# Optimization experiments

Measured on AMD Instinct MI355X. Metric: run time of the kernel, lower is better.

The kernel has to match this reference:

```python
import jax, jax.numpy as jnp
import numpy as np


def setup_inputs() -> dict:
    key = jax.random.key(0)
    ks = jax.random.split(key, 5)
    B, H, S, C, Dh = 2, 16, 2048, 2048, 64
    HID = H * Dh
    return {
        "q": jax.random.normal(ks[0], (B, H, S, Dh), dtype=jnp.float32),
        "k": jax.random.normal(ks[1], (B, H, C + S, Dh), dtype=jnp.float32),
        "v": jax.random.normal(ks[2], (B, H, C + S, Dh), dtype=jnp.float32),
        "memory_length": 256,
        "W": jax.random.normal(ks[3], (HID, HID), dtype=jnp.float32) / np.sqrt(HID),
        "b": jax.random.normal(ks[4], (HID,), dtype=jnp.float32) * 0.01,
    }


def _build_mask(S, KV, memory_length):
    # KV = CACHE_LEN + S; columns >= CACHE_LEN + memory_length are restricted.
    C = KV - S
    rows = jnp.arange(S)[:, None]          # query position in [0, S)
    cols = jnp.arange(KV)[None, :]         # key position in [0, KV)
    restricted = cols >= (C + memory_length)
    # memory rows (< memory_length) never see restricted cols;
    # other rows: strictly-upper-triangular masking (col - (C+mem) > row - mem)
    mem_row = rows < memory_length
    future = (cols - (C + memory_length)) > (rows - memory_length)
    return (restricted & (mem_row | future))  # bool [S, KV], True = masked


def reference(q, k, v, memory_length, W, b):
    B, H, S, Dh = q.shape
    KV = k.shape[2]
    HID = H * Dh
    scale = 1.0 / np.sqrt(Dh).astype(np.float32)
    scores = jnp.einsum('bhsd,bhtd->bhst', q, k) * scale   # [B,H,S,KV]
    mask2d = _build_mask(S, KV, memory_length)             # [S,KV] bool
    scores = jnp.where(mask2d[None, None], -jnp.inf, scores)
    attn_w = jax.nn.softmax(scores, axis=-1)
    attn = jnp.einsum('bhst,bhtd->bshd', attn_w, v).reshape(B, S, HID)
    out = attn @ W.T + b
    # torch module returns full [B,H,S,KV] float mask of 0/1
    mask_full = jnp.broadcast_to(mask2d.astype(q.dtype), (B, H, S, KV))
    return out, mask_full
```

## Files before the change

kernel.cpp:

```cpp
#include <hip/hip_runtime.h>
#include <hip/hip_bf16.h>
#include <math.h>

typedef __bf16 bf16;
typedef __bf16 bf16x4 __attribute__((ext_vector_type(4)));
typedef __bf16 bf16x8 __attribute__((ext_vector_type(8)));
typedef float f32x4 __attribute__((ext_vector_type(4)));

#define MFMA(a, b, c) __builtin_amdgcn_mfma_f32_16x16x32_bf16((a), (b), (c), 0, 0, 0)

constexpr int Bb  = 2;
constexpr int Hh  = 16;
constexpr int Ss  = 2048;
constexpr int KVv = 4096;
constexpr int Dd  = 64;
constexpr int Cc  = KVv - Ss;
constexpr int HID = Hh * Dd;

constexpr float QSCL = 0.125f * 1.44269504088896340736f;

constexpr size_t MASK_F4   = (size_t)Bb * Hh * Ss * KVv / 4;
constexpr size_t SCR_BYTES = 16777216ull + 16777216ull + 2097152ull + 8388608ull;
constexpr size_t M2_F4     = MASK_F4 - (2097152ull + 8388608ull) / 16;
constexpr size_t M1_F4     = 50000000;

__device__ __forceinline__ void write_mask_range(
    float* __restrict__ mout, int mem, size_t lo, size_t hi,
    int mblk, int nmblk, int tid, int nthr)
{
    const int R = Cc + mem;
    const size_t stride = (size_t)nmblk * nthr;
    for (size_t i = lo + (size_t)mblk * nthr + tid; i < hi; i += stride) {
        size_t flat = i * 4;
        int t = (int)(flat & (size_t)(KVv - 1));
        int s = (int)((flat >> 12) & (size_t)(Ss - 1));
        int thr = (s < mem) ? R : (s + Cc + 1);
        f32x4 vv;
        vv[0] = (float)(t >= thr);
        vv[1] = (float)(t + 1 >= thr);
        vv[2] = (float)(t + 2 >= thr);
        vv[3] = (float)(t + 3 >= thr);
        __builtin_nontemporal_store(vv, (f32x4*)(mout + flat));
    }
}

__global__ __launch_bounds__(256) void cvt_kernel(
    const float* __restrict__ K, const float* __restrict__ W,
    bf16* __restrict__ Kb, bf16* __restrict__ Wb)
{
    const size_t nK4 = (size_t)Bb * Hh * KVv * Dd / 4;
    const size_t nW4 = (size_t)HID * HID / 4;
    const size_t total = nK4 + nW4;
    const size_t stride = (size_t)gridDim.x * blockDim.x;
    for (size_t i = (size_t)blockIdx.x * blockDim.x + threadIdx.x; i < total; i += stride) {
        float4 x = (i < nK4) ? ((const float4*)K)[i] : ((const float4*)W)[i - nK4];
        bf16x4 t;
        t[0] = (bf16)x.x; t[1] = (bf16)x.y; t[2] = (bf16)x.z; t[3] = (bf16)x.w;
        if (i < nK4) ((bf16x4*)Kb)[i] = t;
        else         ((bf16x4*)Wb)[i - nK4] = t;
    }
}

__global__ __launch_bounds__(256) void vT_kernel(
    const float* __restrict__ V, bf16* __restrict__ Vt)
{
    __shared__ __align__(16) bf16 T[64][72];
    const int bh = blockIdx.y;
    const int t0 = blockIdx.x * 64;
    const int row = threadIdx.x >> 2;
    const int cg  = threadIdx.x & 3;

    const float* vb = V + (size_t)bh * KVv * Dd + (size_t)(t0 + row) * Dd + cg * 16;
    float4 x0 = ((const float4*)vb)[0];
    float4 x1 = ((const float4*)vb)[1];
    float4 x2 = ((const float4*)vb)[2];
    float4 x3 = ((const float4*)vb)[3];
    float xs[16] = {x0.x,x0.y,x0.z,x0.w, x1.x,x1.y,x1.z,x1.w,
                    x2.x,x2.y,x2.z,x2.w, x3.x,x3.y,x3.z,x3.w};
#pragma unroll
    for (int j = 0; j < 16; ++j)
        T[cg * 16 + j][row] = (bf16)xs[j];
    __syncthreads();

    const int d = row;
    bf16* o = Vt + (size_t)bh * Dd * KVv + (size_t)d * KVv + t0 + cg * 16;
    bf16x8 a0 = *(const bf16x8*)&T[d][cg * 16];
    bf16x8 a1 = *(const bf16x8*)&T[d][cg * 16 + 8];
    ((bf16x8*)o)[0] = a0;
    ((bf16x8*)o)[1] = a1;
}

template <bool MASKED>
__device__ __forceinline__ void kv_tile(
    int t0, const bf16* __restrict__ kb_p, const bf16* __restrict__ vt_p,
    const bf16x8 qa[2], const int thr[4], int tid, int lr, int lg,
    bf16 (*__restrict__ Klds)[72], bf16 (*__restrict__ Vlds)[72],
    bf16 (*__restrict__ Pw)[72], f32x4 acco[4], float lsum[4])
{
    {
        const int row = tid >> 3, c8 = tid & 7;
        bf16x8 kx = *(const bf16x8*)(kb_p + (size_t)(t0 + row) * Dd + c8 * 8);
        bf16x8 vx = *(const bf16x8*)(vt_p + (size_t)row * KVv + t0 + c8 * 8);
        *(bf16x8*)&Klds[row][c8 * 8] = kx;
        *(bf16x8*)&Vlds[row][c8 * 8] = vx;
    }
    __syncthreads();

    f32x4 accs[4];
#pragma unroll
    for (int kg = 0; kg < 4; ++kg) accs[kg] = (f32x4){0.f, 0.f, 0.f, 0.f};
    __builtin_amdgcn_s_setprio(1);
#pragma unroll
    for (int ks = 0; ks < 2; ++ks) {
#pragma unroll
        for (int kg = 0; kg < 4; ++kg) {
            bf16x8 kf = *(const bf16x8*)&Klds[kg * 16 + lr][ks * 32 + lg * 8];
            accs[kg] = MFMA(qa[ks], kf, accs[kg]);
        }
    }
    __builtin_amdgcn_s_setprio(0);

#pragma unroll
    for (int r = 0; r < 4; ++r) {
#pragma unroll
        for (int kg = 0; kg < 4; ++kg) {
            float sl = accs[kg][r];
            if (MASKED) {
                int tcol = t0 + kg * 16 + lr;
                sl = (tcol < thr[r]) ? sl : -1e30f;
            }
            accs[kg][r] = __builtin_amdgcn_exp2f(sl);
        }
        lsum[r] += (accs[0][r] + accs[1][r]) + (accs[2][r] + accs[3][r]);
#pragma unroll
        for (int kg = 0; kg < 4; ++kg)
            Pw[lg * 4 + r][kg * 16 + lr] = (bf16)accs[kg][r];
    }
    asm volatile("s_waitcnt lgkmcnt(0)" ::: "memory");

    __builtin_amdgcn_s_setprio(1);
#pragma unroll
    for (int ks = 0; ks < 2; ++ks) {
        bf16x8 pa = *(const bf16x8*)&Pw[lr][ks * 32 + lg * 8];
#pragma unroll
        for (int dg = 0; dg < 4; ++dg) {
            bf16x8 vf = *(const bf16x8*)&Vlds[dg * 16 + lr][ks * 32 + lg * 8];
            acco[dg] = MFMA(pa, vf, acco[dg]);
        }
    }
    __builtin_amdgcn_s_setprio(0);
    __syncthreads();
}

__global__ __launch_bounds__(512) void fused_attn_kernel(
    const float* __restrict__ q, const bf16* __restrict__ Kb,
    const bf16* __restrict__ Vtb, const int* __restrict__ memp,
    bf16* __restrict__ attnb, float* __restrict__ mout)
{
    __shared__ __align__(16) bf16 Klds[64][72];
    __shared__ __align__(16) bf16 Vlds[64][72];
    __shared__ __align__(16) bf16 Plds[8][16][72];

    const int fid = blockIdx.x;
    const int mem = *memp;
    if (fid >= 512) {
        write_mask_range(mout, mem, 0, M1_F4, fid - 512, gridDim.x - 512,
                         threadIdx.x, 512);
        return;
    }
    const int xcd = fid & 7;
    const int slot = fid >> 3;
    const int qblk = slot & 15;
    const int bh = (slot >> 4) * 8 + xcd;

    const int tid = threadIdx.x;
    const int w  = tid >> 6;
    const int l  = tid & 63;
    const int lr = l & 15;
    const int lg = l >> 4;
    const int q0 = qblk * 128;
    const int R = Cc + mem;

    const float* qp   = q   + (size_t)bh * Ss * Dd;
    const bf16*  kb_p = Kb  + (size_t)bh * KVv * Dd;
    const bf16*  vt_p = Vtb + (size_t)bh * Dd * KVv;

    const int qrow = q0 + w * 16 + lr;
    bf16x8 qa[2];
#pragma unroll
    for (int ks = 0; ks < 2; ++ks) {
        const float* p8 = qp + (size_t)qrow * Dd + ks * 32 + lg * 8;
        float4 x0 = *(const float4*)p8;
        float4 x1 = *(const float4*)(p8 + 4);
        bf16x8 a;
        a[0] = (bf16)(x0.x * QSCL); a[1] = (bf16)(x0.y * QSCL);
        a[2] = (bf16)(x0.z * QSCL); a[3] = (bf16)(x0.w * QSCL);
        a[4] = (bf16)(x1.x * QSCL); a[5] = (bf16)(x1.y * QSCL);
        a[6] = (bf16)(x1.z * QSCL); a[7] = (bf16)(x1.w * QSCL);
        qa[ks] = a;
    }

    int thr[4];
#pragma unroll
    for (int r = 0; r < 4; ++r) {
        int qabs = q0 + w * 16 + lg * 4 + r;
        thr[r] = (qabs < mem) ? R : (qabs + Cc + 1);
    }
    const int qmaxb = q0 + 127;
    int kv_end = (qmaxb < mem) ? R : (qmaxb + Cc + 1);
    if (kv_end > KVv) kv_end = KVv;
    int thr_min = (q0 < mem) ? R : (q0 + Cc + 1);
    int p1_end = thr_min & ~63;
    if (p1_end > kv_end) p1_end = kv_end;

    f32x4 acco[4];
#pragma unroll
    for (int dg = 0; dg < 4; ++dg) acco[dg] = (f32x4){0.f, 0.f, 0.f, 0.f};
    float lsum[4] = {0.f, 0.f, 0.f, 0.f};

    for (int t0 = 0; t0 < p1_end; t0 += 64)
        kv_tile<false>(t0, kb_p, vt_p, qa, thr, tid, lr, lg, Klds, Vlds, Plds[w], acco, lsum);
    for (int t0 = p1_end; t0 < kv_end; t0 += 64)
        kv_tile<true>(t0, kb_p, vt_p, qa, thr, tid, lr, lg, Klds, Vlds, Plds[w], acco, lsum);

    const int b = bh >> 4, h = bh & 15;
#pragma unroll
    for (int r = 0; r < 4; ++r) {
        float s = lsum[r];
        s += __shfl_xor(s, 1);
        s += __shfl_xor(s, 2);
        s += __shfl_xor(s, 4);
        s += __shfl_xor(s, 8);
        float inv = 1.f / s;
        int qabs = q0 + w * 16 + lg * 4 + r;
        bf16* dst = attnb + (size_t)(b * Ss + qabs) * HID + h * Dd;
#pragma unroll
        for (int dg = 0; dg < 4; ++dg)
            dst[dg * 16 + lr] = (bf16)(acco[dg][r] * inv);
    }
}

__global__ __launch_bounds__(256) void fused_proj_kernel(
    const bf16* __restrict__ A, const bf16* __restrict__ Wb,
    const float* __restrict__ bias, float* __restrict__ out,
    const int* __restrict__ memp, float* __restrict__ mout)
{
    __shared__ __align__(16) bf16 Alds[64][72];
    __shared__ __align__(16) bf16 Wlds[64][72];

    const int fid = blockIdx.x;
    if (fid >= 1024) {
        write_mask_range(mout, *memp, M1_F4, M2_F4, fid - 1024, gridDim.x - 1024,
                         threadIdx.x, 256);
        return;
    }
    const int xcd = fid & 7;
    const int slot = fid >> 3;
    const int o0 = ((slot & 1) * 8 + xcd) * 64;
    const int i0 = (slot >> 1) * 64;

    const int tid = threadIdx.x;
    const int w  = tid >> 6;
    const int l  = tid & 63;
    const int lr = l & 15;
    const int lg = l >> 4;

    f32x4 acc[4];
#pragma unroll
    for (int og = 0; og < 4; ++og) acc[og] = (f32x4){0.f, 0.f, 0.f, 0.f};

    for (int kc = 0; kc < HID; kc += 64) {
        const int row = tid >> 2, cg = tid & 3;
        bf16x8 a0 = ((const bf16x8*)(A  + (size_t)(i0 + row) * HID + kc + cg * 16))[0];
        bf16x8 a1 = ((const bf16x8*)(A  + (size_t)(i0 + row) * HID + kc + cg * 16))[1];
        bf16x8 w0 = ((const bf16x8*)(Wb + (size_t)(o0 + row) * HID + kc + cg * 16))[0];
        bf16x8 w1 = ((const bf16x8*)(Wb + (size_t)(o0 + row) * HID + kc + cg * 16))[1];
        *(bf16x8*)&Alds[row][cg * 16]     = a0;
        *(bf16x8*)&Alds[row][cg * 16 + 8] = a1;
        *(bf16x8*)&Wlds[row][cg * 16]     = w0;
        *(bf16x8*)&Wlds[row][cg * 16 + 8] = w1;
        __syncthreads();
        __builtin_amdgcn_s_setprio(1);
#pragma unroll
        for (int ks = 0; ks < 2; ++ks) {
            bf16x8 af = *(const bf16x8*)&Alds[w * 16 + lr][ks * 32 + lg * 8];
#pragma unroll
            for (int og = 0; og < 4; ++og) {
                bf16x8 wf = *(const bf16x8*)&Wlds[og * 16 + lr][ks * 32 + lg * 8];
                acc[og] = MFMA(af, wf, acc[og]);
            }
        }
        __builtin_amdgcn_s_setprio(0);
        __syncthreads();
    }

#pragma unroll
    for (int r = 0; r < 4; ++r) {
        int i = i0 + w * 16 + lg * 4 + r;
#pragma unroll
        for (int og = 0; og < 4; ++og) {
            int o = o0 + og * 16 + lr;
            __builtin_nontemporal_store(acc[og][r] + bias[o], &out[(size_t)i * HID + o]);
        }
    }
}

__global__ __launch_bounds__(256) void mask_tail_kernel(
    float* __restrict__ mout, const int* __restrict__ memp)
{
    write_mask_range(mout, *memp, M2_F4, MASK_F4, blockIdx.x, gridDim.x,
                     threadIdx.x, 256);
}

extern "C" void kernel_launch(void* const* d_in, const int* in_sizes, int n_in,
                              void* d_out, int out_size, void* d_ws, size_t ws_size,
                              hipStream_t stream)
{
    (void)in_sizes; (void)n_in; (void)out_size; (void)d_ws; (void)ws_size;
    const float* q    = (const float*)d_in[0];
    const float* k    = (const float*)d_in[1];
    const float* v    = (const float*)d_in[2];
    const int*   memp = (const int*)d_in[3];
    const float* W    = (const float*)d_in[4];
    const float* bias = (const float*)d_in[5];

    float* out     = (float*)d_out;
    float* maskout = out + (size_t)Bb * Ss * HID;

    char* scr = (char*)maskout + MASK_F4 * 16 - SCR_BYTES;
    bf16* Kbf   = (bf16*)scr;
    bf16* Vtb   = Kbf + (size_t)Bb * Hh * KVv * Dd;
    bf16* Wbf   = Vtb + (size_t)Bb * Hh * KVv * Dd;
    bf16* attnb = Wbf + (size_t)HID * HID;

    cvt_kernel<<<dim3(1024), 256, 0, stream>>>(k, W, Kbf, Wbf);
    vT_kernel<<<dim3(KVv / 64, Bb * Hh), 256, 0, stream>>>(v, Vtb);
    fused_attn_kernel<<<dim3(512 + 1024), 512, 0, stream>>>(q, Kbf, Vtb, memp, attnb, maskout);
    fused_proj_kernel<<<dim3(1024 + 512), 256, 0, stream>>>(attnb, Wbf, bias, out, memp, maskout);
    mask_tail_kernel<<<dim3(256), 256, 0, stream>>>(maskout, memp);
}
```

Baseline: 265.9 us.

## Merge prep kernels, use workspace scratch, and drop mask tail launch

```diff
diff --git a/kernel.cpp b/kernel.cpp
--- a/kernel.cpp
+++ b/kernel.cpp
@@ -22,7 +22,7 @@
 constexpr size_t MASK_F4   = (size_t)Bb * Hh * Ss * KVv / 4;
 constexpr size_t SCR_BYTES = 16777216ull + 16777216ull + 2097152ull + 8388608ull;
 constexpr size_t M2_F4     = MASK_F4 - (2097152ull + 8388608ull) / 16;
-constexpr size_t M1_F4     = 50000000;
+constexpr size_t M1_F4     = 44000000;
 
 __device__ __forceinline__ void write_mask_range(
     float* __restrict__ mout, int mem, size_t lo, size_t hi,
@@ -44,50 +44,46 @@
     }
 }
 
-__global__ __launch_bounds__(256) void cvt_kernel(
+__global__ __launch_bounds__(256) void prep_kernel(
     const float* __restrict__ K, const float* __restrict__ W,
-    bf16* __restrict__ Kb, bf16* __restrict__ Wb)
-{
+    const float* __restrict__ V,
+    bf16* __restrict__ Kb, bf16* __restrict__ Wb, bf16* __restrict__ Vt)
+{
+    const int bid = blockIdx.x;
+    if (bid < 2048) {
+        __shared__ __align__(16) bf16 T[64][72];
+        const int bh = bid >> 6;
+        const int t0 = (bid & 63) * 64;
+        const int row = threadIdx.x >> 2;
+        const int cg  = threadIdx.x & 3;
+        const float* vb = V + (size_t)bh * KVv * Dd + (size_t)(t0 + row) * Dd + cg * 16;
+        float4 x0 = ((const float4*)vb)[0];
+        float4 x1 = ((const float4*)vb)[1];
+        float4 x2 = ((const float4*)vb)[2];
+        float4 x3 = ((const float4*)vb)[3];
+        float xs[16] = {x0.x,x0.y,x0.z,x0.w, x1.x,x1.y,x1.z,x1.w,
+                        x2.x,x2.y,x2.z,x2.w, x3.x,x3.y,x3.z,x3.w};
+#pragma unroll
+        for (int j = 0; j < 16; ++j)
+            T[cg * 16 + j][row] = (bf16)xs[j];
+        __syncthreads();
+        const int d = row;
+        bf16* o = Vt + (size_t)bh * Dd * KVv + (size_t)d * KVv + t0 + cg * 16;
+        ((bf16x8*)o)[0] = *(const bf16x8*)&T[d][cg * 16];
+        ((bf16x8*)o)[1] = *(const bf16x8*)&T[d][cg * 16 + 8];
+        return;
+    }
     const size_t nK4 = (size_t)Bb * Hh * KVv * Dd / 4;
     const size_t nW4 = (size_t)HID * HID / 4;
     const size_t total = nK4 + nW4;
-    const size_t stride = (size_t)gridDim.x * blockDim.x;
-    for (size_t i = (size_t)blockIdx.x * blockDim.x + threadIdx.x; i < total; i += stride) {
+    const size_t stride = (size_t)(gridDim.x - 2048) * 256;
+    for (size_t i = (size_t)(bid - 2048) * 256 + threadIdx.x; i < total; i += stride) {
         float4 x = (i < nK4) ? ((const float4*)K)[i] : ((const float4*)W)[i - nK4];
         bf16x4 t;
         t[0] = (bf16)x.x; t[1] = (bf16)x.y; t[2] = (bf16)x.z; t[3] = (bf16)x.w;
         if (i < nK4) ((bf16x4*)Kb)[i] = t;
         else         ((bf16x4*)Wb)[i - nK4] = t;
     }
-}
-
-__global__ __launch_bounds__(256) void vT_kernel(
-    const float* __restrict__ V, bf16* __restrict__ Vt)
-{
-    __shared__ __align__(16) bf16 T[64][72];
-    const int bh = blockIdx.y;
-    const int t0 = blockIdx.x * 64;
-    const int row = threadIdx.x >> 2;
-    const int cg  = threadIdx.x & 3;
-
-    const float* vb = V + (size_t)bh * KVv * Dd + (size_t)(t0 + row) * Dd + cg * 16;
-    float4 x0 = ((const float4*)vb)[0];
-    float4 x1 = ((const float4*)vb)[1];
-    float4 x2 = ((const float4*)vb)[2];
-    float4 x3 = ((const float4*)vb)[3];
-    float xs[16] = {x0.x,x0.y,x0.z,x0.w, x1.x,x1.y,x1.z,x1.w,
-                    x2.x,x2.y,x2.z,x2.w, x3.x,x3.y,x3.z,x3.w};
-#pragma unroll
-    for (int j = 0; j < 16; ++j)
-        T[cg * 16 + j][row] = (bf16)xs[j];
-    __syncthreads();
-
-    const int d = row;
-    bf16* o = Vt + (size_t)bh * Dd * KVv + (size_t)d * KVv + t0 + cg * 16;
-    bf16x8 a0 = *(const bf16x8*)&T[d][cg * 16];
-    bf16x8 a1 = *(const bf16x8*)&T[d][cg * 16 + 8];
-    ((bf16x8*)o)[0] = a0;
-    ((bf16x8*)o)[1] = a1;
 }
 
 template <bool MASKED>
@@ -243,14 +239,14 @@
 __global__ __launch_bounds__(256) void fused_proj_kernel(
     const bf16* __restrict__ A, const bf16* __restrict__ Wb,
     const float* __restrict__ bias, float* __restrict__ out,
-    const int* __restrict__ memp, float* __restrict__ mout)
+    const int* __restrict__ memp, float* __restrict__ mout, size_t mhi)
 {
     __shared__ __align__(16) bf16 Alds[64][72];
     __shared__ __align__(16) bf16 Wlds[64][72];
 
     const int fid = blockIdx.x;
     if (fid >= 1024) {
-        write_mask_range(mout, *memp, M1_F4, M2_F4, fid - 1024, gridDim.x - 1024,
+        write_mask_range(mout, *memp, M1_F4, mhi, fid - 1024, gridDim.x - 1024,
                          threadIdx.x, 256);
         return;
     }
@@ -316,7 +312,7 @@
                               void* d_out, int out_size, void* d_ws, size_t ws_size,
                               hipStream_t stream)
 {
-    (void)in_sizes; (void)n_in; (void)out_size; (void)d_ws; (void)ws_size;
+    (void)in_sizes; (void)n_in; (void)out_size;
     const float* q    = (const float*)d_in[0];
     const float* k    = (const float*)d_in[1];
     const float* v    = (const float*)d_in[2];
@@ -327,15 +323,19 @@
     float* out     = (float*)d_out;
     float* maskout = out + (size_t)Bb * Ss * HID;
 
-    char* scr = (char*)maskout + MASK_F4 * 16 - SCR_BYTES;
+    const bool use_ws = ws_size >= SCR_BYTES;
+    char* scr = use_ws ? (char*)d_ws
+                       : (char*)maskout + MASK_F4 * 16 - SCR_BYTES;
     bf16* Kbf   = (bf16*)scr;
     bf16* Vtb   = Kbf + (size_t)Bb * Hh * KVv * Dd;
     bf16* Wbf   = Vtb + (size_t)Bb * Hh * KVv * Dd;
     bf16* attnb = Wbf + (size_t)HID * HID;
 
-    cvt_kernel<<<dim3(1024), 256, 0, stream>>>(k, W, Kbf, Wbf);
-    vT_kernel<<<dim3(KVv / 64, Bb * Hh), 256, 0, stream>>>(v, Vtb);
+    const size_t mhi = use_ws ? MASK_F4 : M2_F4;
+
+    prep_kernel<<<dim3(2048 + 1024), 256, 0, stream>>>(k, W, v, Kbf, Wbf, Vtb);
     fused_attn_kernel<<<dim3(512 + 1024), 512, 0, stream>>>(q, Kbf, Vtb, memp, attnb, maskout);
-    fused_proj_kernel<<<dim3(1024 + 512), 256, 0, stream>>>(attnb, Wbf, bias, out, memp, maskout);
-    mask_tail_kernel<<<dim3(256), 256, 0, stream>>>(maskout, memp);
-}
+    fused_proj_kernel<<<dim3(1024 + 512), 256, 0, stream>>>(attnb, Wbf, bias, out, memp, maskout, mhi);
+    if (!use_ws)
+        mask_tail_kernel<<<dim3(256), 256, 0, stream>>>(maskout, memp);
+}
```

New measurement: 268.4 us. About the same (+1.0%).
